# Performance work log

Measured on AMD Instinct MI355X. Metric: run time of the kernel, lower is better.

Reference implementation:

```python
import jax, jax.numpy as jnp
import numpy as np

EPS = 1e-7  # K.epsilon()
SIZE_IN, IN_CAPS, KSIZE, STRIDE, CAPS, ROUTINGS = 14, 32, 3, 2, 32, 3
SIZE_OUT = (SIZE_IN - KSIZE) // STRIDE + 1  # 6
P = SIZE_OUT * SIZE_OUT          # 36 parent positions
C = KSIZE * KSIZE * IN_CAPS      # 288 child capsules per parent


def _child_parent_map():
    idx = []
    valid = range(0, SIZE_IN - KSIZE + 1, STRIDE)
    for row in valid:
        for col in valid:
            for kr in range(KSIZE):
                start = (row + kr) * SIZE_IN + col
                idx.extend(range(start, start + KSIZE))
    return np.asarray(idx, dtype=np.int32).reshape(P, KSIZE * KSIZE)

CPM = _child_parent_map()  # [P, K^2] static gather indices


def _em_routing(in_act, votes, beta_a, beta_v):
    # in_act: [B,P,C,1,1]; votes: [B,P,C,O,16]
    O = CAPS
    rr = jnp.full(votes.shape[:4] + (1,), 1.0 / O, dtype=votes.dtype)
    bv = beta_v.reshape(1, 1, 1, O, 1)
    ba = beta_a.reshape(1, 1, 1, O)
    out_act = means = None
    for i in range(ROUTINGS):
        lambd = 0.01 * (1.0 - 0.95 ** i)
        # ---- M step ----
        rr_scaled = rr * in_act                                   # [B,P,C,O,1]
        rr_sum = jnp.sum(rr_scaled, axis=2, keepdims=True)        # [B,P,1,O,1]
        means = jnp.sum(rr_scaled * votes, axis=2, keepdims=True) / (rr_sum + EPS)  # [B,P,1,O,16]
        std = jnp.sqrt(jnp.sum(rr_scaled * jnp.square(votes - means), axis=2, keepdims=True) / (rr_sum + EPS))
        costs = bv + jnp.log(std + EPS) * rr_sum                  # [B,P,1,O,16]
        out_act = jax.nn.sigmoid(lambd * (ba - jnp.sum(costs, axis=-1)))[..., None]  # [B,P,1,O,1]
        # ---- E step ----
        if i < ROUTINGS - 1:
            prob_exp = -jnp.sum(jnp.square(votes - means) / (2.0 * jnp.square(std) + EPS), axis=-1, keepdims=True)
            prob_main = -jnp.sum(jnp.log(std + EPS), axis=-1, keepdims=True)
            zz = jnp.log(out_act + EPS) + prob_main + prob_exp   # [B,P,C,O,1]
            rr = jax.nn.softmax(zz, axis=3)
    return out_act, means


def setup_inputs() -> dict:
    key = jax.random.key(0)
    k1, k2, k3, k4, k5 = jax.random.split(key, 5)
    B = 8
    return {
        "in_act": jax.random.uniform(k1, (B, SIZE_IN, SIZE_IN, IN_CAPS, 1), dtype=jnp.float32),
        "in_pose": jax.random.normal(k2, (B, SIZE_IN, SIZE_IN, IN_CAPS, 4, 4), dtype=jnp.float32),
        "W": jax.random.normal(k3, (1, 1, C, CAPS, 4, 4), dtype=jnp.float32) * 0.1,
        "beta_a": jax.random.normal(k4, (CAPS,), dtype=jnp.float32),
        "beta_v": jax.random.normal(k5, (CAPS,), dtype=jnp.float32),
    }


def reference(in_act, in_pose, W, beta_a, beta_v):
    B = in_act.shape[0]
    act = in_act.reshape(B, SIZE_IN * SIZE_IN, IN_CAPS)
    pose = in_pose.reshape(B, SIZE_IN * SIZE_IN, IN_CAPS, 4, 4)
    # gather children for each parent window -> [B,P,C,...]
    act_g = act[:, CPM].reshape(B, P, C, 1, 1)
    pose_g = pose[:, CPM].reshape(B, P, C, 4, 4)
    # votes[b,p,c,o,i,j] = sum_k pose_g[b,p,c,i,k] * W[c,o,k,j]
    votes = jnp.einsum('bpcik,cokj->bpcoij', pose_g, W.reshape(C, CAPS, 4, 4))
    votes = votes.reshape(B, P, C, CAPS, 16)
    out_act, out_pose = _em_routing(act_g, votes, beta_a, beta_v)
    out_act = out_act.reshape(B, SIZE_OUT, SIZE_OUT, CAPS, 1)
    out_pose = out_pose.reshape(B, SIZE_OUT, SIZE_OUT, CAPS, 4, 4)
    return out_act, out_pose
```

## Files before the change

### kernel.cpp

```cpp
#include <hip/hip_runtime.h>
#include <math.h>

#define EPS 1e-7f

constexpr int SIZE_IN = 14;
constexpr int P_  = 36;
constexpr int Cc  = 288;
constexpr int O_  = 32;
constexpr int THREADS = 256;

struct __align__(16) SMem {
    float pose[Cc * 16];
    float act[Cc];
    float red[4][O_][33];
    float mean[O_][17];
    float iv[O_][17];
    float zb[O_];
};

#define F4_TO_ARR(dst, off, f4) \
    dst[(off)+0] = (f4).x; dst[(off)+1] = (f4).y; dst[(off)+2] = (f4).z; dst[(off)+3] = (f4).w;

template<bool HASE, bool LAST>
__device__ __forceinline__ void em_pass(
    SMem& sm, const float* __restrict__ W,
    const float* __restrict__ beta_a, const float* __restrict__ beta_v,
    float lambda, int bp, float* __restrict__ out)
{
    const int tid = threadIdx.x;
    const int o  = tid & 31;
    const int ci = tid >> 5;

    float m[16], iv[16], zb = 0.f;
    if (HASE) {
        #pragma unroll
        for (int j = 0; j < 16; ++j) { m[j] = sm.mean[o][j]; iv[j] = sm.iv[o][j]; }
        zb = sm.zb[o];
    }

    float S0 = 0.f, S1[16], S2[16];
    #pragma unroll
    for (int j = 0; j < 16; ++j) { S1[j] = 0.f; S2[j] = 0.f; }

    const float4* wp0 = reinterpret_cast<const float4*>(W + (size_t)(ci * O_ + o) * 16);
    float4 nw0 = wp0[0], nw1 = wp0[1], nw2 = wp0[2], nw3 = wp0[3];
    const float4* pp0 = reinterpret_cast<const float4*>(&sm.pose[ci * 16]);
    float4 np0 = pp0[0], np1 = pp0[1], np2 = pp0[2], np3 = pp0[3];

    #pragma unroll 2
    for (int t = 0; t < 36; ++t) {
        const int c = t * 8 + ci;
        float w[16], q[16];
        F4_TO_ARR(w, 0, nw0) F4_TO_ARR(w, 4, nw1) F4_TO_ARR(w, 8, nw2) F4_TO_ARR(w, 12, nw3)
        F4_TO_ARR(q, 0, np0) F4_TO_ARR(q, 4, np1) F4_TO_ARR(q, 8, np2) F4_TO_ARR(q, 12, np3)
        if (t + 1 < 36) {
            const int cn = c + 8;
            const float4* wn = reinterpret_cast<const float4*>(W + (size_t)(cn * O_ + o) * 16);
            nw0 = wn[0]; nw1 = wn[1]; nw2 = wn[2]; nw3 = wn[3];
            const float4* pn = reinterpret_cast<const float4*>(&sm.pose[cn * 16]);
            np0 = pn[0]; np1 = pn[1]; np2 = pn[2]; np3 = pn[3];
        }

        float v[16];
        #pragma unroll
        for (int i = 0; i < 4; ++i) {
            #pragma unroll
            for (int jj = 0; jj < 4; ++jj) {
                float acc = q[i*4+0] * w[0*4+jj];
                acc = fmaf(q[i*4+1], w[1*4+jj], acc);
                acc = fmaf(q[i*4+2], w[2*4+jj], acc);
                acc = fmaf(q[i*4+3], w[3*4+jj], acc);
                v[i*4+jj] = acc;
            }
        }

        float ws;
        if (HASE) {
            float s = 0.f;
            #pragma unroll
            for (int j = 0; j < 16; ++j) { float d = v[j] - m[j]; s = fmaf(d * d, iv[j], s); }
            float zz = zb - s;
            float mx = zz;
            #pragma unroll
            for (int k = 16; k; k >>= 1) mx = fmaxf(mx, __shfl_xor(mx, k));
            float e = __expf(zz - mx);
            float sum = e;
            #pragma unroll
            for (int k = 16; k; k >>= 1) sum += __shfl_xor(sum, k);
            float rr = e / sum;
            ws = rr * sm.act[c];
        } else {
            ws = sm.act[c] * (1.0f / 32.0f);
        }

        S0 += ws;
        #pragma unroll
        for (int j = 0; j < 16; ++j) {
            float t0 = ws * v[j];
            S1[j] += t0;
            S2[j] = fmaf(t0, v[j], S2[j]);
        }
    }

    S0 += __shfl_xor(S0, 32);
    #pragma unroll
    for (int j = 0; j < 16; ++j) {
        S1[j] += __shfl_xor(S1[j], 32);
        S2[j] += __shfl_xor(S2[j], 32);
    }
    if (!(tid & 32)) {
        const int wv = tid >> 6;
        float* r = sm.red[wv][o];
        r[0] = S0;
        #pragma unroll
        for (int j = 0; j < 16; ++j) { r[1 + j] = S1[j]; r[17 + j] = S2[j]; }
    }
    __syncthreads();

    if (tid < O_) {
        const float* r0 = sm.red[0][tid];
        const float* r1 = sm.red[1][tid];
        const float* r2 = sm.red[2][tid];
        const float* r3 = sm.red[3][tid];
        float s0 = r0[0] + r1[0] + r2[0] + r3[0];
        float denom = s0 + EPS;
        float sumlog = 0.f;
        float mm[16];
        #pragma unroll
        for (int j = 0; j < 16; ++j) {
            float s1 = r0[1+j] + r1[1+j] + r2[1+j] + r3[1+j];
            float s2 = r0[17+j] + r1[17+j] + r2[17+j] + r3[17+j];
            float mj = s1 / denom;
            float varn = fmaxf(s2 - 2.f * mj * s1 + mj * mj * s0, 0.f);
            float sd = sqrtf(varn / denom);
            mm[j] = mj;
            sumlog += __logf(sd + EPS);
            if (!LAST) {
                sm.mean[tid][j] = mj;
                sm.iv[tid][j] = 1.f / (fmaf(2.f * sd, sd, EPS));
            }
        }
        float cost = fmaf(16.f, beta_v[tid], s0 * sumlog);
        float oact = 1.f / (1.f + __expf(-(lambda * (beta_a[tid] - cost))));
        if (!LAST) {
            sm.zb[tid] = __logf(oact + EPS) - sumlog;
        } else {
            out[bp * O_ + tid] = oact;
            float* po = out + 8 * P_ * O_ + (size_t)(bp * O_ + tid) * 16;
            #pragma unroll
            for (int j = 0; j < 16; ++j) po[j] = mm[j];
        }
    }
    __syncthreads();
}

__global__ __launch_bounds__(THREADS, 2) void convcaps_kernel(
    const float* __restrict__ in_act, const float* __restrict__ in_pose,
    const float* __restrict__ W, const float* __restrict__ beta_a,
    const float* __restrict__ beta_v, float* __restrict__ out)
{
    __shared__ SMem sm;
    const int bp = blockIdx.x;
    const int b  = bp / P_;
    const int p  = bp % P_;
    const int tid = threadIdx.x;
    const int row0 = (p / 6) * 2, col0 = (p % 6) * 2;

    for (int f = tid; f < 9 * 128; f += THREADS) {
        const int qw = f >> 7, r = f & 127;
        const int pix = (row0 + qw / 3) * SIZE_IN + (col0 + qw % 3);
        reinterpret_cast<float4*>(sm.pose)[qw * 128 + r] =
            reinterpret_cast<const float4*>(in_pose + (size_t)(b * 196 + pix) * 512)[r];
    }
    for (int idx = tid; idx < Cc; idx += THREADS) {
        const int qw = idx >> 5, ic = idx & 31;
        const int pix = (row0 + qw / 3) * SIZE_IN + (col0 + qw % 3);
        sm.act[idx] = in_act[(size_t)(b * 196 + pix) * 32 + ic];
    }
    __syncthreads();

    em_pass<false, false>(sm, W, beta_a, beta_v, 0.0f,      bp, out);
    em_pass<true,  false>(sm, W, beta_a, beta_v, 0.0005f,   bp, out);
    em_pass<true,  true >(sm, W, beta_a, beta_v, 0.000975f, bp, out);
}

extern "C" void kernel_launch(void* const* d_in, const int* in_sizes, int n_in,
                              void* d_out, int out_size, void* d_ws, size_t ws_size,
                              hipStream_t stream) {
    const float* in_act  = (const float*)d_in[0];
    const float* in_pose = (const float*)d_in[1];
    const float* W       = (const float*)d_in[2];
    const float* beta_a  = (const float*)d_in[3];
    const float* beta_v  = (const float*)d_in[4];
    float* out = (float*)d_out;

    convcaps_kernel<<<dim3(8 * P_), dim3(THREADS), 0, stream>>>(
        in_act, in_pose, W, beta_a, beta_v, out);
}
```

Before: 162.0 us.

## Double block threads and parallelize per-capsule finalize across 512 threads

New measurement: 315.2 us. 94.6% more time.

```diff
diff --git a/kernel.cpp b/kernel.cpp
--- a/kernel.cpp
+++ b/kernel.cpp
@@ -7,12 +7,15 @@
 constexpr int P_  = 36;
 constexpr int Cc  = 288;
 constexpr int O_  = 32;
-constexpr int THREADS = 256;
+constexpr int THREADS = 512;
+constexpr int CI = THREADS / O_;
+constexpr int NT = Cc / CI;
+constexpr int NW = THREADS / 64;
 
 struct __align__(16) SMem {
     float pose[Cc * 16];
     float act[Cc];
-    float red[4][O_][33];
+    float red[NW][O_][33];
     float mean[O_][17];
     float iv[O_][17];
     float zb[O_];
@@ -48,13 +51,13 @@
     float4 np0 = pp0[0], np1 = pp0[1], np2 = pp0[2], np3 = pp0[3];
 
     #pragma unroll 2
-    for (int t = 0; t < 36; ++t) {
-        const int c = t * 8 + ci;
+    for (int t = 0; t < NT; ++t) {
+        const int c = t * CI + ci;
         float w[16], q[16];
         F4_TO_ARR(w, 0, nw0) F4_TO_ARR(w, 4, nw1) F4_TO_ARR(w, 8, nw2) F4_TO_ARR(w, 12, nw3)
         F4_TO_ARR(q, 0, np0) F4_TO_ARR(q, 4, np1) F4_TO_ARR(q, 8, np2) F4_TO_ARR(q, 12, np3)
-        if (t + 1 < 36) {
-            const int cn = c + 8;
+        if (t + 1 < NT) {
+            const int cn = c + CI;
             const float4* wn = reinterpret_cast<const float4*>(W + (size_t)(cn * O_ + o) * 16);
             nw0 = wn[0]; nw1 = wn[1]; nw2 = wn[2]; nw3 = wn[3];
             const float4* pn = reinterpret_cast<const float4*>(&sm.pose[cn * 16]);
@@ -117,44 +120,44 @@
     }
     __syncthreads();
 
-    if (tid < O_) {
-        const float* r0 = sm.red[0][tid];
-        const float* r1 = sm.red[1][tid];
-        const float* r2 = sm.red[2][tid];
-        const float* r3 = sm.red[3][tid];
-        float s0 = r0[0] + r1[0] + r2[0] + r3[0];
+    {
+        const int of = tid >> 4, jf = tid & 15;
+        float s0 = 0.f, s1 = 0.f, s2 = 0.f;
+        #pragma unroll
+        for (int w = 0; w < NW; ++w) {
+            s0 += sm.red[w][of][0];
+            s1 += sm.red[w][of][1 + jf];
+            s2 += sm.red[w][of][17 + jf];
+        }
         float denom = s0 + EPS;
-        float sumlog = 0.f;
-        float mm[16];
-        #pragma unroll
-        for (int j = 0; j < 16; ++j) {
-            float s1 = r0[1+j] + r1[1+j] + r2[1+j] + r3[1+j];
-            float s2 = r0[17+j] + r1[17+j] + r2[17+j] + r3[17+j];
-            float mj = s1 / denom;
-            float varn = fmaxf(s2 - 2.f * mj * s1 + mj * mj * s0, 0.f);
-            float sd = sqrtf(varn / denom);
-            mm[j] = mj;
-            sumlog += __logf(sd + EPS);
-            if (!LAST) {
-                sm.mean[tid][j] = mj;
-                sm.iv[tid][j] = 1.f / (fmaf(2.f * sd, sd, EPS));
+        float mj = s1 / denom;
+        float varn = fmaxf(s2 - 2.f * mj * s1 + mj * mj * s0, 0.f);
+        float sd = sqrtf(varn / denom);
+        float lg = __logf(sd + EPS);
+        float sumlog = lg;
+        #pragma unroll
+        for (int k = 1; k < 16; k <<= 1) sumlog += __shfl_xor(sumlog, k);
+        if (!LAST) {
+            sm.mean[of][jf] = mj;
+            sm.iv[of][jf] = 1.f / fmaf(2.f * sd, sd, EPS);
+            if (jf == 0) {
+                float cost = fmaf(16.f, beta_v[of], s0 * sumlog);
+                float oact = 1.f / (1.f + __expf(-(lambda * (beta_a[of] - cost))));
+                sm.zb[of] = __logf(oact + EPS) - sumlog;
             }
-        }
-        float cost = fmaf(16.f, beta_v[tid], s0 * sumlog);
-        float oact = 1.f / (1.f + __expf(-(lambda * (beta_a[tid] - cost))));
-        if (!LAST) {
-            sm.zb[tid] = __logf(oact + EPS) - sumlog;
         } else {
-            out[bp * O_ + tid] = oact;
-            float* po = out + 8 * P_ * O_ + (size_t)(bp * O_ + tid) * 16;
-            #pragma unroll
-            for (int j = 0; j < 16; ++j) po[j] = mm[j];
+            out[8 * P_ * O_ + (size_t)(bp * O_ + of) * 16 + jf] = mj;
+            if (jf == 0) {
+                float cost = fmaf(16.f, beta_v[of], s0 * sumlog);
+                float oact = 1.f / (1.f + __expf(-(lambda * (beta_a[of] - cost))));
+                out[bp * O_ + of] = oact;
+            }
         }
     }
     __syncthreads();
 }
 
-__global__ __launch_bounds__(THREADS, 2) void convcaps_kernel(
+__global__ __launch_bounds__(THREADS, 4) void convcaps_kernel(
     const float* __restrict__ in_act, const float* __restrict__ in_pose,
     const float* __restrict__ W, const float* __restrict__ beta_a,
     const float* __restrict__ beta_v, float* __restrict__ out)
```
